# Kernel optimization log

Measured on AMD Instinct MI355X. Metric: run time of the kernel, lower is better.

Reference implementation:

```python
import jax, jax.numpy as jnp
import numpy as np

B, S, D, FF, E, K = 4, 2048, 1024, 4096, 16, 2
EPS = 1e-6
MOE_SCALING = 1.0


def setup_inputs() -> dict:
    key = jax.random.key(0)
    k0, k1, k2, k3 = jax.random.split(key, 4)
    hidden_states = jax.random.normal(k0, (B, S, D), jnp.float32)
    ln_weight = jnp.ones((D,), jnp.float32)
    gate_w = jax.random.normal(k1, (D, E), jnp.float32) * 0.02
    gate_b = jnp.zeros((E,), jnp.float32)
    wi = jax.random.normal(k2, (E, D, FF), jnp.float32) * (1.0 / np.sqrt(D).astype(np.float32))
    wo = jax.random.normal(k3, (E, FF, D), jnp.float32) * (1.0 / np.sqrt(FF).astype(np.float32))
    return {"hidden_states": hidden_states, "ln_weight": ln_weight,
            "gate_w": gate_w, "gate_b": gate_b, "wi": wi, "wo": wo}


def reference(hidden_states, ln_weight, gate_w, gate_b, wi, wo):
    # --- T5LayerNorm (RMS norm, no mean subtraction, no bias) ---
    var = jnp.mean(hidden_states * hidden_states, axis=-1, keepdims=True)
    norm_x = hidden_states * jax.lax.rsqrt(var + EPS) * ln_weight

    T = B * S
    xt = norm_x.reshape(T, D)  # tokens

    # --- NaiveGate: linear -> top-k -> softmax over selected logits ---
    logits = xt @ gate_w + gate_b                      # [T, E]
    top_vals, top_idx = jax.lax.top_k(logits, K)       # [T, K]
    scores = jax.nn.softmax(top_vals, axis=-1)         # [T, K]
    # dense combine weights [T, E] (zero for non-selected experts)
    combine = jnp.zeros((T, E), xt.dtype).at[jnp.arange(T)[:, None], top_idx].add(scores)

    # --- expert FFNs (T5DenseReluDense per expert), combined by gate weight ---
    def body(acc, xs):
        w_i, w_o, c = xs                               # [D,FF], [FF,D], [T]
        h = jax.nn.relu(xt @ w_i)                      # [T, FF]
        return acc + c[:, None] * (h @ w_o), None

    y0 = jnp.zeros((T, D), xt.dtype)
    y, _ = jax.lax.scan(body, y0, (wi, wo, combine.T))

    y = MOE_SCALING * y
    # dropout is identity at eval; scaled residual add
    layer_output = hidden_states + y.reshape(B, S, D)
    return layer_output
```

## Files before the change

kernel.cpp:

```cpp
#include <hip/hip_runtime.h>

#define T_TOK 8192
#define DIM   1024
#define FFD   4096
#define NEXP  16

typedef __bf16 bf16_t;
typedef bf16_t bf16x4 __attribute__((ext_vector_type(4)));
typedef bf16_t bf16x8 __attribute__((ext_vector_type(8)));
typedef float  f32x4  __attribute__((ext_vector_type(4)));

__device__ __forceinline__ void gload_lds16(const void* g, void* l) {
  __builtin_amdgcn_global_load_lds((__attribute__((address_space(1))) void*)(g),
                                   (__attribute__((address_space(3))) void*)(l),
                                   16, 0, 0);
}

__global__ __launch_bounds__(256) void k_norm_gate(
    const float* __restrict__ x, const float* __restrict__ lnw,
    const float* __restrict__ gw, const float* __restrict__ gb,
    bf16_t* __restrict__ xt, int* __restrict__ cnt,
    int* __restrict__ stok, float* __restrict__ swgt,
    int* __restrict__ tslot)
{
  const int t = blockIdx.x;
  const int tid = threadIdx.x;
  const int wave = tid >> 6, lane = tid & 63;

  float4 v = ((const float4*)(x + (size_t)t * DIM))[tid];
  float ss = v.x*v.x + v.y*v.y + v.z*v.z + v.w*v.w;
  #pragma unroll
  for (int off = 32; off > 0; off >>= 1) ss += __shfl_down(ss, off, 64);

  __shared__ float red[4];
  __shared__ float racc[4][16];
  __shared__ int   sel[2];
  __shared__ float swv[2];
  if (lane == 0) red[wave] = ss;
  __syncthreads();
  float r = rsqrtf((red[0]+red[1]+red[2]+red[3]) * (1.0f/DIM) + 1e-6f);

  float4 lw = ((const float4*)lnw)[tid];
  float nv[4];
  nv[0] = v.x*r*lw.x; nv[1] = v.y*r*lw.y; nv[2] = v.z*r*lw.z; nv[3] = v.w*r*lw.w;
  bf16x4 nb; nb[0]=(bf16_t)nv[0]; nb[1]=(bf16_t)nv[1]; nb[2]=(bf16_t)nv[2]; nb[3]=(bf16_t)nv[3];
  ((bf16x4*)(xt + (size_t)t * DIM))[tid] = nb;

  float acc[16];
  #pragma unroll
  for (int e=0;e<16;e++) acc[e]=0.f;
  #pragma unroll
  for (int j=0;j<4;j++){
    const float4* row = (const float4*)(gw + ((size_t)(tid*4+j))*16);
    #pragma unroll
    for (int q=0;q<4;q++){
      float4 g = row[q];
      acc[q*4+0] += nv[j]*g.x;
      acc[q*4+1] += nv[j]*g.y;
      acc[q*4+2] += nv[j]*g.z;
      acc[q*4+3] += nv[j]*g.w;
    }
  }
  #pragma unroll
  for (int e=0;e<16;e++){
    #pragma unroll
    for (int off=32;off>0;off>>=1) acc[e] += __shfl_down(acc[e], off, 64);
  }
  if (lane==0){
    #pragma unroll
    for (int e=0;e<16;e++) racc[wave][e]=acc[e];
  }
  __syncthreads();
  if (tid==0){
    float lg[16];
    #pragma unroll
    for (int e=0;e<16;e++) lg[e] = racc[0][e]+racc[1][e]+racc[2][e]+racc[3][e] + gb[e];
    int i0=0; float v0=lg[0];
    for (int e=1;e<16;e++) if (lg[e]>v0){v0=lg[e]; i0=e;}
    int i1=-1; float v1=-3.4e38f;
    for (int e=0;e<16;e++) if (e!=i0 && lg[e]>v1){v1=lg[e]; i1=e;}
    float ex = expf(v1-v0);
    float s0 = 1.0f/(1.0f+ex);
    float s1 = ex * s0;
    sel[0]=i0; sel[1]=i1; swv[0]=s0; swv[1]=s1;
  }
  __syncthreads();
  if (tid<2){
    int ii = sel[tid]; float sv = swv[tid];
    int p = atomicAdd(&cnt[ii],1);
    stok[ii*T_TOK+p]=t; swgt[ii*T_TOK+p]=sv;
    tslot[2*t+tid] = (ii<<16) | p;
  }
}

__global__ void k_offsets(const int* __restrict__ cnt, int* __restrict__ offs){
  if (threadIdx.x==0){
    int s=0;
    for (int e=0;e<NEXP;e++){ offs[e]=s; s+=cnt[e]; }
    offs[NEXP]=s;
  }
}

__global__ __launch_bounds__(256) void k_transpose2(
    const float* __restrict__ wi, bf16_t* __restrict__ wiT,
    const float* __restrict__ wo, bf16_t* __restrict__ woT)
{
  __shared__ bf16_t lds[64*64];
  const int z = blockIdx.z;
  const float* in; bf16_t* out; int R, C, bx, by, e;
  if (z < NEXP){ in=wi; out=wiT; R=DIM; C=FFD; e=z;
                 bx=blockIdx.x; by=blockIdx.y; }
  else        { in=wo; out=woT; R=FFD; C=DIM; e=z-NEXP;
                 bx=blockIdx.x & 15; by=blockIdx.y + 16*(blockIdx.x>>4); }
  const int r0 = by*64, c0 = bx*64;
  const int tid = threadIdx.x;

  {
    const int rr = tid >> 4;
    const int c4 = (tid & 15) * 4;
    const float* src = in + ((size_t)e*R + r0 + rr)*C + c0 + c4;
    #pragma unroll
    for (int i=0;i<4;i++){
      int rrow = rr + i*16;
      float4 vv = *(const float4*)(src + (size_t)i*16*C);
      bf16x4 b; b[0]=(bf16_t)vv.x; b[1]=(bf16_t)vv.y; b[2]=(bf16_t)vv.z; b[3]=(bf16_t)vv.w;
      int swz = ((rrow >> 3) & 7) << 3;
      *(bf16x4*)(lds + rrow*64 + (c4 ^ swz)) = b;
    }
  }
  __syncthreads();
  {
    const int r8  = (tid & 7) * 8;
    const int cc  = tid >> 3;
    const int swz = (tid & 7) << 3;
    #pragma unroll
    for (int i=0;i<2;i++){
      int c = cc + i*32;
      bf16x8 b;
      #pragma unroll
      for (int j=0;j<8;j++) b[j] = lds[(r8+j)*64 + (c ^ swz)];
      *(bf16x8*)(out + ((size_t)e*C + c0 + c)*R + r0 + r8) = b;
    }
  }
}

template<int KD, bool G1>
__global__ __launch_bounds__(256) void k_gemm(
    const bf16_t* __restrict__ A0, const bf16_t* __restrict__ Bt,
    const int* __restrict__ cnt, const int* __restrict__ offs,
    const int* __restrict__ stok, const float* __restrict__ swgt,
    bf16_t* __restrict__ Hout, float* __restrict__ Out)
{
  const int e  = blockIdx.z;
  const int cn = cnt[e];
  const int m0 = blockIdx.y * 128;
  if (m0 >= cn) return;
  const int n0 = blockIdx.x * 128;
  const int oe = offs[e];
  constexpr int NR = G1 ? FFD : DIM;

  __shared__ bf16_t As[128*64];
  __shared__ bf16_t Bs[128*64];

  const int tid  = threadIdx.x;
  const int wave = tid >> 6, lane = tid & 63;
  const int lrow = lane >> 3;
  const int lcol = (((lane & 7) ^ lrow) * 8);

  const bf16_t* aptr[4];
  const bf16_t* bptr[4];
  #pragma unroll
  for (int j=0;j<4;j++){
    int chunk = wave*4 + j;
    int r = chunk*8 + lrow;
    int grow = m0 + r;
    if constexpr (G1){
      int tok = (grow < cn) ? stok[e*T_TOK + grow] : 0;
      aptr[j] = A0 + (size_t)tok*KD + lcol;
    } else {
      aptr[j] = A0 + (size_t)(oe + grow)*KD + lcol;
    }
    bptr[j] = Bt + ((size_t)e*NR + (n0 + r))*KD + lcol;
  }

  f32x4 acc[4][4];
  #pragma unroll
  for (int mt=0;mt<4;mt++)
    #pragma unroll
    for (int nt=0;nt<4;nt++)
      #pragma unroll
      for (int q=0;q<4;q++) acc[mt][nt][q]=0.f;

  const int wm = wave & 1, wn = wave >> 1;
  const bf16_t* aslds = As + ((wm*64) + (lane & 15))*64;
  const bf16_t* bslds = Bs + ((wn*64) + (lane & 15))*64;
  const int swz0 = ((((lane>>4) + 0) ^ (lane & 7)) * 8);
  const int swz1 = ((((lane>>4) + 4) ^ (lane & 7)) * 8);

  for (int k0=0; k0<KD; k0+=64){
    #pragma unroll
    for (int j=0;j<4;j++){
      gload_lds16(aptr[j] + k0, As + (wave*4+j)*512);
      gload_lds16(bptr[j] + k0, Bs + (wave*4+j)*512);
    }
    __syncthreads();
    #pragma unroll
    for (int kc=0;kc<64;kc+=32){
      const int swz = (kc == 0) ? swz0 : swz1;
      bf16x8 af[4], bfr[4];
      #pragma unroll
      for (int mt=0;mt<4;mt++) af[mt]  = *(const bf16x8*)(aslds + mt*1024 + swz);
      #pragma unroll
      for (int nt=0;nt<4;nt++) bfr[nt] = *(const bf16x8*)(bslds + nt*1024 + swz);
      #pragma unroll
      for (int mt=0;mt<4;mt++)
        #pragma unroll
        for (int nt=0;nt<4;nt++)
          acc[mt][nt] = __builtin_amdgcn_mfma_f32_16x16x32_bf16(af[mt], bfr[nt], acc[mt][nt], 0, 0, 0);
    }
    __syncthreads();
  }

  const int lq = lane >> 4;
  const int lc = lane & 15;
  #pragma unroll
  for (int mt=0;mt<4;mt++){
    #pragma unroll
    for (int i=0;i<4;i++){
      int rl = wm*64 + mt*16 + lq*4 + i;
      int grow = m0 + rl;
      if (grow < cn){
        if constexpr (G1){
          float w = swgt[e*T_TOK + grow];
          size_t hbase = (size_t)(oe + grow) * FFD;
          #pragma unroll
          for (int nt=0;nt<4;nt++){
            int colg = n0 + wn*64 + nt*16 + lc;
            float vv = acc[mt][nt][i];
            vv = vv > 0.f ? vv * w : 0.f;
            Hout[hbase + colg] = (bf16_t)vv;
          }
        } else {
          size_t obase = (size_t)(oe + grow) * DIM;
          #pragma unroll
          for (int nt=0;nt<4;nt++){
            int colg = n0 + wn*64 + nt*16 + lc;
            Out[obase + colg] = acc[mt][nt][i];
          }
        }
      }
    }
  }
}

__global__ __launch_bounds__(256) void k_combine(
    const float* __restrict__ hidden, const float* __restrict__ y2,
    const int* __restrict__ offs, const int* __restrict__ tslot,
    float* __restrict__ out)
{
  const int t = blockIdx.x;
  const int tid = threadIdx.x;
  const int s0 = tslot[2*t+0], s1 = tslot[2*t+1];
  const size_t r0 = (size_t)(offs[s0>>16] + (s0 & 0xffff));
  const size_t r1 = (size_t)(offs[s1>>16] + (s1 & 0xffff));
  float4 a = ((const float4*)(hidden + (size_t)t*DIM))[tid];
  float4 b = ((const float4*)(y2 + r0*DIM))[tid];
  float4 c = ((const float4*)(y2 + r1*DIM))[tid];
  a.x += b.x + c.x;
  a.y += b.y + c.y;
  a.z += b.z + c.z;
  a.w += b.w + c.w;
  ((float4*)(out + (size_t)t*DIM))[tid] = a;
}

extern "C" void kernel_launch(void* const* d_in, const int* in_sizes, int n_in,
                              void* d_out, int out_size, void* d_ws, size_t ws_size,
                              hipStream_t stream) {
  const float* hidden = (const float*)d_in[0];
  const float* lnw    = (const float*)d_in[1];
  const float* gw     = (const float*)d_in[2];
  const float* gb     = (const float*)d_in[3];
  const float* wi     = (const float*)d_in[4];
  const float* wo     = (const float*)d_in[5];
  float* out = (float*)d_out;

  char* ws = (char*)d_ws;
  size_t o = 0;
  auto alloc = [&](size_t bytes)->char*{ char* p = ws + o; o += (bytes + 255) & ~(size_t)255; return p; };
  bf16_t* xt   = (bf16_t*)alloc((size_t)T_TOK*DIM*2);
  bf16_t* wiT  = (bf16_t*)alloc((size_t)NEXP*FFD*DIM*2);
  bf16_t* woT  = (bf16_t*)alloc((size_t)NEXP*DIM*FFD*2);
  bf16_t* h    = (bf16_t*)alloc((size_t)(2*T_TOK + 128)*FFD*2);
  int*    stok = (int*)alloc((size_t)NEXP*T_TOK*4);
  float*  swgt = (float*)alloc((size_t)NEXP*T_TOK*4);
  int*    tslot= (int*)alloc((size_t)2*T_TOK*4);
  int*    cnt  = (int*)alloc(256);
  int*    offs = (int*)alloc(256);
  (void)ws_size; (void)in_sizes; (void)n_in; (void)out_size;

  float* y2 = (float*)wiT;

  hipMemsetAsync(cnt, 0, 64, stream);

  k_norm_gate<<<dim3(T_TOK), 256, 0, stream>>>(hidden, lnw, gw, gb, xt, cnt, stok, swgt, tslot);
  k_offsets<<<dim3(1), 64, 0, stream>>>(cnt, offs);
  k_transpose2<<<dim3(64, 16, 2*NEXP), 256, 0, stream>>>(wi, wiT, wo, woT);
  k_gemm<DIM, true ><<<dim3(FFD/128, T_TOK/128, NEXP), 256, 0, stream>>>(xt, wiT, cnt, offs, stok, swgt, h, nullptr);
  k_gemm<FFD, false><<<dim3(DIM/128, T_TOK/128, NEXP), 256, 0, stream>>>(h,  woT, cnt, offs, stok, swgt, nullptr, y2);
  k_combine<<<dim3(T_TOK), 256, 0, stream>>>(hidden, y2, offs, tslot, out);
}
```

Before: 1.212 ms.

## Use 256x256 tiles with 512 threads and double-buffered LDS in first expert GEMM

```diff
diff --git a/kernel.cpp b/kernel.cpp
--- a/kernel.cpp
+++ b/kernel.cpp
@@ -145,22 +145,28 @@
 }
 
 template<int KD, bool G1>
-__global__ __launch_bounds__(256) void k_gemm(
+__global__ __launch_bounds__(G1?512:256, 2) void k_gemm(
     const bf16_t* __restrict__ A0, const bf16_t* __restrict__ Bt,
     const int* __restrict__ cnt, const int* __restrict__ offs,
     const int* __restrict__ stok, const float* __restrict__ swgt,
     bf16_t* __restrict__ Hout, float* __restrict__ Out)
 {
+  constexpr int BM = G1 ? 256 : 128;
+  constexpr int BN = G1 ? 256 : 128;
+  constexpr int MT = G1 ? 8 : 4;
+  constexpr int NT = 4;
+  constexpr int NK = KD / 64;
+  constexpr int NR = G1 ? FFD : DIM;
+
   const int e  = blockIdx.z;
   const int cn = cnt[e];
-  const int m0 = blockIdx.y * 128;
+  const int m0 = blockIdx.y * BM;
   if (m0 >= cn) return;
-  const int n0 = blockIdx.x * 128;
+  const int n0 = blockIdx.x * BN;
   const int oe = offs[e];
-  constexpr int NR = G1 ? FFD : DIM;
-
-  __shared__ bf16_t As[128*64];
-  __shared__ bf16_t Bs[128*64];
+
+  __shared__ bf16_t As[2][BM*64];
+  __shared__ bf16_t Bs[2][BN*64];
 
   const int tid  = threadIdx.x;
   const int wave = tid >> 6, lane = tid & 63;
@@ -183,39 +189,46 @@
     bptr[j] = Bt + ((size_t)e*NR + (n0 + r))*KD + lcol;
   }
 
-  f32x4 acc[4][4];
-  #pragma unroll
-  for (int mt=0;mt<4;mt++)
-    #pragma unroll
-    for (int nt=0;nt<4;nt++)
+  auto stage = [&](int buf, int kof){
+    #pragma unroll
+    for (int j=0;j<4;j++){
+      gload_lds16(aptr[j] + kof, &As[buf][(wave*4+j)*512]);
+      gload_lds16(bptr[j] + kof, &Bs[buf][(wave*4+j)*512]);
+    }
+  };
+
+  f32x4 acc[MT][NT];
+  #pragma unroll
+  for (int mt=0;mt<MT;mt++)
+    #pragma unroll
+    for (int nt=0;nt<NT;nt++)
       #pragma unroll
       for (int q=0;q<4;q++) acc[mt][nt][q]=0.f;
 
   const int wm = wave & 1, wn = wave >> 1;
-  const bf16_t* aslds = As + ((wm*64) + (lane & 15))*64;
-  const bf16_t* bslds = Bs + ((wn*64) + (lane & 15))*64;
   const int swz0 = ((((lane>>4) + 0) ^ (lane & 7)) * 8);
   const int swz1 = ((((lane>>4) + 4) ^ (lane & 7)) * 8);
 
-  for (int k0=0; k0<KD; k0+=64){
-    #pragma unroll
-    for (int j=0;j<4;j++){
-      gload_lds16(aptr[j] + k0, As + (wave*4+j)*512);
-      gload_lds16(bptr[j] + k0, Bs + (wave*4+j)*512);
-    }
-    __syncthreads();
+  stage(0, 0);
+  __syncthreads();
+
+  for (int kt=0; kt<NK; ++kt){
+    if (kt+1 < NK) stage((kt+1)&1, (kt+1)*64);
+    const int cur = kt & 1;
+    const bf16_t* aslds = &As[cur][(wm*(BM/2) + (lane & 15))*64];
+    const bf16_t* bslds = &Bs[cur][(wn*64     + (lane & 15))*64];
     #pragma unroll
     for (int kc=0;kc<64;kc+=32){
       const int swz = (kc == 0) ? swz0 : swz1;
-      bf16x8 af[4], bfr[4];
-      #pragma unroll
-      for (int mt=0;mt<4;mt++) af[mt]  = *(const bf16x8*)(aslds + mt*1024 + swz);
-      #pragma unroll
-      for (int nt=0;nt<4;nt++) bfr[nt] = *(const bf16x8*)(bslds + nt*1024 + swz);
-      #pragma unroll
-      for (int mt=0;mt<4;mt++)
+      bf16x8 af[MT], bfr[NT];
+      #pragma unroll
+      for (int mt=0;mt<MT;mt++) af[mt]  = *(const bf16x8*)(aslds + mt*1024 + swz);
+      #pragma unroll
+      for (int nt=0;nt<NT;nt++) bfr[nt] = *(const bf16x8*)(bslds + nt*1024 + swz);
+      #pragma unroll
+      for (int mt=0;mt<MT;mt++)
         #pragma unroll
-        for (int nt=0;nt<4;nt++)
+        for (int nt=0;nt<NT;nt++)
           acc[mt][nt] = __builtin_amdgcn_mfma_f32_16x16x32_bf16(af[mt], bfr[nt], acc[mt][nt], 0, 0, 0);
     }
     __syncthreads();
@@ -224,17 +237,17 @@
   const int lq = lane >> 4;
   const int lc = lane & 15;
   #pragma unroll
-  for (int mt=0;mt<4;mt++){
+  for (int mt=0;mt<MT;mt++){
     #pragma unroll
     for (int i=0;i<4;i++){
-      int rl = wm*64 + mt*16 + lq*4 + i;
+      int rl = wm*(BM/2) + mt*16 + lq*4 + i;
       int grow = m0 + rl;
       if (grow < cn){
         if constexpr (G1){
           float w = swgt[e*T_TOK + grow];
           size_t hbase = (size_t)(oe + grow) * FFD;
           #pragma unroll
-          for (int nt=0;nt<4;nt++){
+          for (int nt=0;nt<NT;nt++){
             int colg = n0 + wn*64 + nt*16 + lc;
             float vv = acc[mt][nt][i];
             vv = vv > 0.f ? vv * w : 0.f;
@@ -243,7 +256,7 @@
         } else {
           size_t obase = (size_t)(oe + grow) * DIM;
           #pragma unroll
-          for (int nt=0;nt<4;nt++){
+          for (int nt=0;nt<NT;nt++){
             int colg = n0 + wn*64 + nt*16 + lc;
             Out[obase + colg] = acc[mt][nt][i];
           }
@@ -290,7 +303,7 @@
   bf16_t* xt   = (bf16_t*)alloc((size_t)T_TOK*DIM*2);
   bf16_t* wiT  = (bf16_t*)alloc((size_t)NEXP*FFD*DIM*2);
   bf16_t* woT  = (bf16_t*)alloc((size_t)NEXP*DIM*FFD*2);
-  bf16_t* h    = (bf16_t*)alloc((size_t)(2*T_TOK + 128)*FFD*2);
+  bf16_t* h    = (bf16_t*)alloc((size_t)(2*T_TOK + 256)*FFD*2);
   int*    stok = (int*)alloc((size_t)NEXP*T_TOK*4);
   float*  swgt = (float*)alloc((size_t)NEXP*T_TOK*4);
   int*    tslot= (int*)alloc((size_t)2*T_TOK*4);
@@ -305,7 +318,7 @@
   k_norm_gate<<<dim3(T_TOK), 256, 0, stream>>>(hidden, lnw, gw, gb, xt, cnt, stok, swgt, tslot);
   k_offsets<<<dim3(1), 64, 0, stream>>>(cnt, offs);
   k_transpose2<<<dim3(64, 16, 2*NEXP), 256, 0, stream>>>(wi, wiT, wo, woT);
-  k_gemm<DIM, true ><<<dim3(FFD/128, T_TOK/128, NEXP), 256, 0, stream>>>(xt, wiT, cnt, offs, stok, swgt, h, nullptr);
+  k_gemm<DIM, true ><<<dim3(FFD/256, T_TOK/256, NEXP), 512, 0, stream>>>(xt, wiT, cnt, offs, stok, swgt, h, nullptr);
   k_gemm<FFD, false><<<dim3(DIM/128, T_TOK/128, NEXP), 256, 0, stream>>>(h,  woT, cnt, offs, stok, swgt, nullptr, y2);
   k_combine<<<dim3(T_TOK), 256, 0, stream>>>(hidden, y2, offs, tslot, out);
 }
```

Result: no change. 1.191 ms (-1.7%).
